# Optimization experiments

Measured on AMD Instinct MI355X. Metric: run time of the kernel, lower is better.

Reference implementation:

```python
import jax, jax.numpy as jnp
import numpy as np
from jax import lax

B, T = 2, 2048
HID = 2048
H, K, KC = 16, 128, 4
D = H * K  # projection dim
EPS = 1e-5
SCALE = K ** -0.5


def causal_conv_silu(x, w, b):
    # x: [B,T,D], depthwise causal conv, w: [D,KC], b: [D]
    xp = jnp.pad(jnp.swapaxes(x, 1, 2), ((0, 0), (0, 0), (KC - 1, 0)))  # [B,D,T+KC-1]
    y = lax.conv_general_dilated(xp, w[:, None, :], (1,), 'VALID', feature_group_count=D)
    return jax.nn.silu(jnp.swapaxes(y, 1, 2) + b)


def l2norm(x):
    return x * lax.rsqrt(jnp.sum(x * x, -1, keepdims=True) + 1e-6)


def kda_scan(q, k, v, g, beta):
    # gated delta-rule linear recurrence (KDA), per-key-dim log decay g
    # q,k,v,g: [B,T,H,K]; beta: [B,T,H]
    qT, kT, vT, gT, bT = (jnp.moveaxis(a, 1, 0) for a in (q, k, v, g, beta))
    S0 = jnp.zeros((q.shape[0], H, K, K), q.dtype)  # state [B,H,K,V]

    def step(S, inp):
        qt, kt, vt, gt, bt = inp
        S = S * jnp.exp(gt)[..., None]                                   # decay along K
        vd = (vt - jnp.einsum('bhkv,bhk->bhv', S, kt)) * bt[..., None]   # delta-rule error * beta
        S = S + kt[..., None] * vd[:, :, None, :]                        # rank-1 update
        return S, jnp.einsum('bhkv,bhk->bhv', S, qt)

    _, o = lax.scan(step, S0, (qT, kT, vT, gT, bT))
    return jnp.moveaxis(o, 0, 1)  # [B,T,H,K]


def _forward(x, Wq, Wk, Wv, conv_q_w, conv_q_b, conv_k_w, conv_k_b, conv_v_w, conv_v_b,
             Wfa, Wfb, A_log, dt_bias, Wb, Wga, Wgb, o_norm_w, Wo):
    b, t = x.shape[:2]
    q = causal_conv_silu(x @ Wq, conv_q_w, conv_q_b).reshape(b, t, H, K)
    k = causal_conv_silu(x @ Wk, conv_k_w, conv_k_b).reshape(b, t, H, K)
    v = causal_conv_silu(x @ Wv, conv_v_w, conv_v_b).reshape(b, t, H, K)
    # fine-grained decay gate: g = -exp(A_log[h]) * softplus(f_b(f_a(x)) + dt_bias)
    g = jax.nn.softplus((x @ Wfa) @ Wfb + dt_bias).reshape(b, t, H, K)
    g = -jnp.exp(A_log)[None, None, :, None] * g
    beta = jax.nn.sigmoid(x @ Wb)  # [B,T,H]
    q = l2norm(q) * SCALE
    k = l2norm(k)
    o = kda_scan(q, k, v, g, beta)  # [B,T,H,K]
    # gated head-wise RMSNorm
    gate = ((x @ Wga) @ Wgb).reshape(b, t, H, K)
    var = jnp.mean(o * o, -1, keepdims=True)
    o = o * lax.rsqrt(var + EPS) * o_norm_w * jax.nn.sigmoid(gate)
    return o.reshape(b, t, D) @ Wo


def setup_inputs() -> dict:
    key = jax.random.key(0)
    ks = jax.random.split(key, 16)
    s = 0.02
    f32 = jnp.float32
    return {
        'x': jax.random.normal(ks[0], (B, T, HID), f32),
        'Wq': jax.random.normal(ks[1], (HID, D), f32) * s,
        'Wk': jax.random.normal(ks[2], (HID, D), f32) * s,
        'Wv': jax.random.normal(ks[3], (HID, D), f32) * s,
        'conv_q_w': jax.random.normal(ks[4], (D, KC), f32) * 0.2,
        'conv_q_b': jnp.zeros((D,), f32),
        'conv_k_w': jax.random.normal(ks[5], (D, KC), f32) * 0.2,
        'conv_k_b': jnp.zeros((D,), f32),
        'conv_v_w': jax.random.normal(ks[6], (D, KC), f32) * 0.2,
        'conv_v_b': jnp.zeros((D,), f32),
        'Wfa': jax.random.normal(ks[7], (HID, K), f32) * s,
        'Wfb': jax.random.normal(ks[8], (K, D), f32) * s,
        'A_log': jnp.log(jax.random.uniform(ks[9], (H,), f32, 1.0, 16.0)),
        'dt_bias': jnp.zeros((D,), f32),
        'Wb': jax.random.normal(ks[10], (HID, H), f32) * s,
        'Wga': jax.random.normal(ks[11], (HID, K), f32) * s,
        'Wgb': jax.random.normal(ks[12], (K, D), f32) * s,
        'o_norm_w': jnp.ones((K,), f32),
        'Wo': jax.random.normal(ks[13], (D, HID), f32) * s,
    }


def reference(x, Wq, Wk, Wv, conv_q_w, conv_q_b, conv_k_w, conv_k_b, conv_v_w, conv_v_b,
              Wfa, Wfb, A_log, dt_bias, Wb, Wga, Wgb, o_norm_w, Wo):
    return _forward(x, Wq, Wk, Wv, conv_q_w, conv_q_b, conv_k_w, conv_k_b, conv_v_w, conv_v_b,
                    Wfa, Wfb, A_log, dt_bias, Wb, Wga, Wgb, o_norm_w, Wo)
```

## Files before the change

kernel.cpp:

```cpp
#include <hip/hip_runtime.h>
#include <cstddef>

#define Bsz 2
#define Tt  2048
#define HIDc 2048
#define Hh  16
#define Kc  128
#define Dc  2048
#define BT  (Bsz*Tt)
#define TS  8
#define FGBs 384

typedef __attribute__((ext_vector_type(8))) __bf16 bf16x8;
typedef __attribute__((ext_vector_type(4))) __bf16 bf16x4;
typedef __attribute__((ext_vector_type(4))) float f32x4;

__device__ __forceinline__ float epilogue(float vacc, int c, int mode,
                                          const float* __restrict__ alog,
                                          const float* __restrict__ dtb) {
    if (mode == 1) {
        float z  = vacc + dtb[c];
        float sp = fmaxf(z, 0.f) + log1pf(expf(-fabsf(z)));
        return expf(-expf(alog[c >> 7]) * sp);
    } else if (mode == 3) {
        return (c >= 256) ? 1.f / (1.f + expf(-vacc)) : vacc;
    }
    return vacc;
}

__global__ __launch_bounds__(256) void gemm_bf16_mfma(
    const __bf16* __restrict__ AB, size_t az,
    const __bf16* __restrict__ BwB, size_t bz,
    float* __restrict__ CB, size_t cz, __bf16* __restrict__ C2,
    int M, int N, int K, int lda, int mode,
    const float* __restrict__ alog, const float* __restrict__ dtb)
{
    __shared__ __bf16 As[128 * 64];
    __shared__ __bf16 Bs[128 * 64];
    const __bf16* A = AB + (size_t)blockIdx.z * az;
    const __bf16* Bw = BwB + (size_t)blockIdx.z * bz;
    float* C = CB + (size_t)blockIdx.z * cz;
    if (mode == 5) mode = (blockIdx.z == 0) ? 1 : 0;
    const int tid = threadIdx.x;
    const int lane = tid & 63;
    const int wave = tid >> 6;
    const int wr = wave >> 1, wc = wave & 1;
    const int l15 = lane & 15, g = lane >> 4;
    const int row0 = blockIdx.y * 128, col0 = blockIdx.x * 128;

    f32x4 acc[4][4];
#pragma unroll
    for (int m = 0; m < 4; m++)
#pragma unroll
        for (int n = 0; n < 4; n++)
            acc[m][n] = (f32x4){0.f, 0.f, 0.f, 0.f};

    for (int k0 = 0; k0 < K; k0 += 64) {
        __syncthreads();
#pragma unroll
        for (int i = 0; i < 4; i++) {
            const int c = i * 256 + tid;
            const int row = c >> 3, kc = c & 7;
            const int scol = k0 + 8 * (kc ^ (row & 7));
            __builtin_amdgcn_global_load_lds(
                (const __attribute__((address_space(1))) void*)(A + (size_t)(row0 + row) * lda + scol),
                (__attribute__((address_space(3))) void*)(As + (size_t)(i * 256 + (tid & ~63)) * 8),
                16, 0, 0);
        }
#pragma unroll
        for (int i = 0; i < 4; i++) {
            const int c = i * 256 + tid;
            const int row = c >> 3, kc = c & 7;
            const int scol = k0 + 8 * (kc ^ (row & 7));
            __builtin_amdgcn_global_load_lds(
                (const __attribute__((address_space(1))) void*)(Bw + (size_t)(col0 + row) * K + scol),
                (__attribute__((address_space(3))) void*)(Bs + (size_t)(i * 256 + (tid & ~63)) * 8),
                16, 0, 0);
        }
        __syncthreads();
#pragma unroll
        for (int ks = 0; ks < 2; ks++) {
            bf16x8 af[4], bfr[4];
#pragma unroll
            for (int m = 0; m < 4; m++) {
                const int row = wr * 64 + m * 16 + l15;
                const int kc = ks * 4 + g;
                af[m] = *(const bf16x8*)(As + row * 64 + 8 * (kc ^ (row & 7)));
            }
#pragma unroll
            for (int n = 0; n < 4; n++) {
                const int col = wc * 64 + n * 16 + l15;
                const int kc = ks * 4 + g;
                bfr[n] = *(const bf16x8*)(Bs + col * 64 + 8 * (kc ^ (col & 7)));
            }
#pragma unroll
            for (int m = 0; m < 4; m++)
#pragma unroll
                for (int n = 0; n < 4; n++)
                    acc[m][n] = __builtin_amdgcn_mfma_f32_16x16x32_bf16(
                        af[m], bfr[n], acc[m][n], 0, 0, 0);
        }
    }
#pragma unroll
    for (int m = 0; m < 4; m++) {
        const int rbase = row0 + wr * 64 + m * 16 + g * 4;
#pragma unroll
        for (int n = 0; n < 4; n++) {
            const int col = col0 + wc * 64 + n * 16 + l15;
#pragma unroll
            for (int r = 0; r < 4; r++) {
                const float val = epilogue(acc[m][n][r], col, mode, alog, dtb);
                C[(size_t)(rbase + r) * N + col] = val;
                if (C2) C2[(size_t)(rbase + r) * N + col] = (__bf16)val;
            }
        }
    }
}

__global__ __launch_bounds__(256) void cvt_bf16(
    const float* __restrict__ in, __bf16* __restrict__ o)
{
    const int i = blockIdx.x * 256 + threadIdx.x;
    float4 v = *(const float4*)(in + (size_t)4 * i);
    bf16x4 r;
    r[0] = (__bf16)v.x; r[1] = (__bf16)v.y; r[2] = (__bf16)v.z; r[3] = (__bf16)v.w;
    *(bf16x4*)(o + (size_t)4 * i) = r;
}

__global__ __launch_bounds__(256) void transpose_to_bf16(
    const float* __restrict__ W, __bf16* __restrict__ WT, int Kd, int N)
{
    __shared__ float tile[32][33];
    const int n0 = blockIdx.x * 32, k0 = blockIdx.y * 32;
    const int tx = threadIdx.x & 31, ty = threadIdx.x >> 5;
#pragma unroll
    for (int i = 0; i < 4; i++)
        tile[ty + 8 * i][tx] = W[(size_t)(k0 + ty + 8 * i) * N + n0 + tx];
    __syncthreads();
#pragma unroll
    for (int i = 0; i < 4; i++)
        WT[(size_t)(n0 + ty + 8 * i) * Kd + k0 + tx] = (__bf16)tile[tx][ty + 8 * i];
}

__global__ __launch_bounds__(256) void transpose3_to_bf16(
    const float* __restrict__ W0, const float* __restrict__ W1,
    const float* __restrict__ W2, __bf16* __restrict__ WTB, size_t wz,
    int Kd, int N)
{
    __shared__ float tile[32][33];
    const float* W = (blockIdx.z == 0) ? W0 : (blockIdx.z == 1) ? W1 : W2;
    __bf16* WT = WTB + (size_t)blockIdx.z * wz;
    const int n0 = blockIdx.x * 32, k0 = blockIdx.y * 32;
    const int tx = threadIdx.x & 31, ty = threadIdx.x >> 5;
#pragma unroll
    for (int i = 0; i < 4; i++)
        tile[ty + 8 * i][tx] = W[(size_t)(k0 + ty + 8 * i) * N + n0 + tx];
    __syncthreads();
#pragma unroll
    for (int i = 0; i < 4; i++)
        WT[(size_t)(n0 + ty + 8 * i) * Kd + k0 + tx] = (__bf16)tile[tx][ty + 8 * i];
}

__global__ __launch_bounds__(256) void pack_fgbT(
    const float* __restrict__ Wfa, const float* __restrict__ Wga,
    const float* __restrict__ Wb, __bf16* __restrict__ BcatT)
{
    const int i = blockIdx.x * 256 + threadIdx.x;
    if (i >= FGBs * HIDc) return;
    const int c = i / HIDc, k = i % HIDc;
    float v = 0.f;
    if (c < 128)      v = Wfa[(size_t)k * 128 + c];
    else if (c < 256) v = Wga[(size_t)k * 128 + (c - 128)];
    else if (c < 272) v = Wb[(size_t)k * 16 + (c - 256)];
    BcatT[i] = (__bf16)v;
}

__global__ __launch_bounds__(128) void conv_silu_norm(
    const float* __restrict__ pre, const float* __restrict__ cw,
    const float* __restrict__ cb, float* __restrict__ out, int mode)
{
    const int bid = blockIdx.x;
    const int h = bid & (Hh - 1);
    const int bt = bid >> 4;
    const int t = bt & (Tt - 1);
    const int lane = threadIdx.x;
    const int col = h * Kc + lane;
    const float w0 = cw[col * 4 + 0], w1 = cw[col * 4 + 1];
    const float w2 = cw[col * 4 + 2], w3 = cw[col * 4 + 3];
    const float* bp = pre + (size_t)bt * Dc + col;
    float acc = cb[col] + w3 * bp[0];
    if (t >= 1) acc += w2 * bp[-Dc];
    if (t >= 2) acc += w1 * bp[-2 * Dc];
    if (t >= 3) acc += w0 * bp[-3 * Dc];
    float val = acc / (1.f + expf(-acc));
    if (mode) {
        float ss = val * val;
#pragma unroll
        for (int m = 1; m < 64; m <<= 1) ss += __shfl_xor(ss, m);
        __shared__ float p2[2];
        if ((lane & 63) == 0) p2[lane >> 6] = ss;
        __syncthreads();
        float tot = p2[0] + p2[1];
        float r = rsqrtf(tot + 1e-6f);
        val *= r;
        if (mode == 2) val *= 0.08838834764831845f;
    }
    out[(size_t)bt * Dc + col] = val;
}

template <int CTRL>
__device__ __forceinline__ float dpp_add(float v) {
    return __int_as_float(__builtin_amdgcn_update_dpp(
        0, __float_as_int(v), CTRL, 0xf, 0xf, true));
}

__device__ __forceinline__ void reduce3_row(float& a, float& b, float& c) {
    a += dpp_add<0xB1>(a);
    b += dpp_add<0xB1>(b);
    c += dpp_add<0xB1>(c);
    a += dpp_add<0x4E>(a);
    b += dpp_add<0x4E>(b);
    c += dpp_add<0x4E>(c);
    a += dpp_add<0x124>(a);
    b += dpp_add<0x124>(b);
    c += dpp_add<0x124>(c);
    a += dpp_add<0x128>(a);
    b += dpp_add<0x128>(b);
    c += dpp_add<0x128>(c);
}

__device__ __forceinline__ float kda_step(
    const float4 cq[2], const float4 ck[2], const float4 cd[2],
    float cv, float cbt, float S[8])
{
    float kv0 = 0.f, kv1 = 0.f, qs0 = 0.f, qs1 = 0.f, qk0 = 0.f, qk1 = 0.f;
#pragma unroll
    for (int i = 0; i < 2; i++) {
        S[4 * i + 0] *= cd[i].x;
        S[4 * i + 1] *= cd[i].y;
        S[4 * i + 2] *= cd[i].z;
        S[4 * i + 3] *= cd[i].w;
        kv0 = fmaf(ck[i].x, S[4 * i + 0], kv0);
        kv1 = fmaf(ck[i].y, S[4 * i + 1], kv1);
        kv0 = fmaf(ck[i].z, S[4 * i + 2], kv0);
        kv1 = fmaf(ck[i].w, S[4 * i + 3], kv1);
        qs0 = fmaf(cq[i].x, S[4 * i + 0], qs0);
        qs1 = fmaf(cq[i].y, S[4 * i + 1], qs1);
        qs0 = fmaf(cq[i].z, S[4 * i + 2], qs0);
        qs1 = fmaf(cq[i].w, S[4 * i + 3], qs1);
        qk0 = fmaf(ck[i].x, cq[i].x, qk0);
        qk1 = fmaf(ck[i].y, cq[i].y, qk1);
        qk0 = fmaf(ck[i].z, cq[i].z, qk0);
        qk1 = fmaf(ck[i].w, cq[i].w, qk1);
    }
    float kv = kv0 + kv1, qs = qs0 + qs1, qk = qk0 + qk1;
    reduce3_row(kv, qs, qk);
    float vd = (cv - kv) * cbt;
    float ov = fmaf(qk, vd, qs);
#pragma unroll
    for (int i = 0; i < 2; i++) {
        S[4 * i + 0] = fmaf(ck[i].x, vd, S[4 * i + 0]);
        S[4 * i + 1] = fmaf(ck[i].y, vd, S[4 * i + 1]);
        S[4 * i + 2] = fmaf(ck[i].z, vd, S[4 * i + 2]);
        S[4 * i + 3] = fmaf(ck[i].w, vd, S[4 * i + 3]);
    }
    return ov;
}

__device__ __forceinline__ void kda_tile(
    const float (*sm)[TS * 128], const float* vm,
    const float* bm, float S[8], int sl0, int sl1, int vloc,
    float* __restrict__ op, int lane)
{
    float4 cq[2], ck[2], cd[2];
    float cv, cb;
    cq[0] = *(const float4*)&sm[0][sl0];
    ck[0] = *(const float4*)&sm[1][sl0];
    cd[0] = *(const float4*)&sm[2][sl0];
    cq[1] = *(const float4*)&sm[0][sl1];
    ck[1] = *(const float4*)&sm[1][sl1];
    cd[1] = *(const float4*)&sm[2][sl1];
    cv = vm[vloc];
    cb = bm[0];
#pragma unroll
    for (int t = 0; t < TS; ++t) {
        float4 nq[2], nk[2], nd[2];
        float nv = 0.f, nb = 0.f;
        if (t + 1 < TS) {
            nq[0] = *(const float4*)&sm[0][(t + 1) * 128 + sl0];
            nk[0] = *(const float4*)&sm[1][(t + 1) * 128 + sl0];
            nd[0] = *(const float4*)&sm[2][(t + 1) * 128 + sl0];
            nq[1] = *(const float4*)&sm[0][(t + 1) * 128 + sl1];
            nk[1] = *(const float4*)&sm[1][(t + 1) * 128 + sl1];
            nd[1] = *(const float4*)&sm[2][(t + 1) * 128 + sl1];
            nv = vm[(t + 1) * 4 + vloc];
            nb = bm[t + 1];
        }
        const float ov = kda_step(cq, ck, cd, cv, cb, S);
        if ((lane & 15) == 0)
            op[(size_t)t * Dc + vloc] = ov;
        if (t + 1 < TS) {
#pragma unroll
            for (int i = 0; i < 2; i++) { cq[i] = nq[i]; ck[i] = nk[i]; cd[i] = nd[i]; }
            cv = nv; cb = nb;
        }
    }
}

__global__ __launch_bounds__(64, 2) void kda_scan_kernel(
    const float* __restrict__ q, const float* __restrict__ k,
    const float* __restrict__ v, const float* __restrict__ dec,
    const float* __restrict__ fgb, float* __restrict__ o)
{
    __shared__ float sA[3][TS * 128];
    __shared__ float sB[3][TS * 128];
    __shared__ float sC[3][TS * 128];
    __shared__ float vA[TS * 4], vB[TS * 4], vC[TS * 4];
    __shared__ float bA[TS], bB[TS], bC[TS];

    const int bid = blockIdx.x;
    const int r8 = bid & 7;
    const int s = bid >> 3;
    const int bh = r8 + 8 * (s >> 5);
    const int vc = s & 31;
    const int h = bh & (Hh - 1);
    const int b = bh >> 4;
    const int lane = threadIdx.x;
    const int vloc = lane >> 4;
    const int kq = lane & 15;
    const int sl0 = ((kq * 2 + 0 + vloc) & 31) * 4;
    const int sl1 = ((kq * 2 + 1 + vloc) & 31) * 4;
    const size_t base = ((size_t)b * Tt) * Dc + h * Kc;
    const size_t bbase = ((size_t)b * Tt) * FGBs + 256 + h;

    float S[8];
#pragma unroll
    for (int i = 0; i < 8; i++) S[i] = 0.f;

    const int s_t = lane >> 5;
    const int s_w = lane & 31;

#define STAGE(TILE, SM, VM, BM)                                                 \
    {                                                                           \
        _Pragma("unroll")                                                       \
        for (int r = 0; r < 4; r++) {                                           \
            const size_t rb = base + (size_t)((TILE) * TS + 2 * r + s_t) * Dc   \
                              + s_w * 4;                                        \
            __builtin_amdgcn_global_load_lds(                                   \
                (const __attribute__((address_space(1))) void*)(q + rb),        \
                (__attribute__((address_space(3))) void*)(&SM[0][r * 256]),     \
                16, 0, 0);                                                      \
            __builtin_amdgcn_global_load_lds(                                   \
                (const __attribute__((address_space(1))) void*)(k + rb),        \
                (__attribute__((address_space(3))) void*)(&SM[1][r * 256]),     \
                16, 0, 0);                                                      \
            __builtin_amdgcn_global_load_lds(                                   \
                (const __attribute__((address_space(1))) void*)(dec + rb),      \
                (__attribute__((address_space(3))) void*)(&SM[2][r * 256]),     \
                16, 0, 0);                                                      \
        }                                                                       \
        if (lane < 32)                                                          \
            __builtin_amdgcn_global_load_lds(                                   \
                (const __attribute__((address_space(1))) void*)(v + base        \
                    + (size_t)((TILE) * TS + (lane >> 2)) * Dc + vc * 4         \
                    + (lane & 3)),                                              \
                (__attribute__((address_space(3))) void*)(&VM[0]), 4, 0, 0);    \
        if (lane < TS)                                                          \
            __builtin_amdgcn_global_load_lds(                                   \
                (const __attribute__((address_space(1))) void*)(fgb + bbase     \
                    + (size_t)((TILE) * TS + lane) * FGBs),                     \
                (__attribute__((address_space(3))) void*)(&BM[0]), 4, 0, 0);    \
    }

    STAGE(0, sA, vA, bA);
    STAGE(1, sB, vB, bB);
    asm volatile("s_waitcnt vmcnt(14)" ::: "memory");
    __builtin_amdgcn_sched_barrier(0);

    const int NT = Tt / TS;
    int cur = 0, nx2 = 2;
    for (int tile = 0; tile < NT; ++tile) {
        if (tile + 2 < NT) {
            float (*sT)[TS * 128] = (nx2 == 0) ? sA : (nx2 == 1) ? sB : sC;
            float* vT = (nx2 == 0) ? vA : (nx2 == 1) ? vB : vC;
            float* bT = (nx2 == 0) ? bA : (nx2 == 1) ? bB : bC;
            STAGE(tile + 2, sT, vT, bT);
            __builtin_amdgcn_sched_barrier(0);
        }
        const float (*sm)[TS * 128] = (cur == 0) ? sA : (cur == 1) ? sB : sC;
        const float* vm = (cur == 0) ? vA : (cur == 1) ? vB : vC;
        const float* bm = (cur == 0) ? bA : (cur == 1) ? bB : bC;
        kda_tile(sm, vm, bm, S, sl0, sl1, vloc,
                 o + base + (size_t)tile * TS * Dc + vc * 4, lane);
        if (tile + 2 < NT)
            asm volatile("s_waitcnt vmcnt(22)" ::: "memory");
        else
            asm volatile("s_waitcnt vmcnt(8)" ::: "memory");
        __builtin_amdgcn_sched_barrier(0);
        cur = (cur == 2) ? 0 : cur + 1;
        nx2 = (nx2 == 2) ? 0 : nx2 + 1;
    }
#undef STAGE
}

__global__ __launch_bounds__(128) void post_norm(
    const float* __restrict__ o, const float* __restrict__ gate,
    const float* __restrict__ onw, __bf16* __restrict__ og)
{
    const int bid = blockIdx.x;
    const int h = bid & (Hh - 1);
    const int bt = bid >> 4;
    const int lane = threadIdx.x;
    size_t idx = (size_t)bt * Dc + h * Kc + lane;
    float ov = o[idx];
    float ss = ov * ov;
#pragma unroll
    for (int m = 1; m < 64; m <<= 1) ss += __shfl_xor(ss, m);
    __shared__ float p2[2];
    if ((lane & 63) == 0) p2[lane >> 6] = ss;
    __syncthreads();
    float var = (p2[0] + p2[1]) * (1.f / 128.f);
    float r = rsqrtf(var + 1e-5f);
    float gt = gate[idx];
    og[idx] = (__bf16)(ov * r * onw[lane] * (1.f / (1.f + expf(-gt))));
}

extern "C" void kernel_launch(void* const* d_in, const int* in_sizes, int n_in,
                              void* d_out, int out_size, void* d_ws, size_t ws_size,
                              hipStream_t stream) {
    const float* x        = (const float*)d_in[0];
    const float* Wq       = (const float*)d_in[1];
    const float* Wk       = (const float*)d_in[2];
    const float* Wv       = (const float*)d_in[3];
    const float* conv_q_w = (const float*)d_in[4];
    const float* conv_q_b = (const float*)d_in[5];
    const float* conv_k_w = (const float*)d_in[6];
    const float* conv_k_b = (const float*)d_in[7];
    const float* conv_v_w = (const float*)d_in[8];
    const float* conv_v_b = (const float*)d_in[9];
    const float* Wfa      = (const float*)d_in[10];
    const float* Wfb      = (const float*)d_in[11];
    const float* A_log    = (const float*)d_in[12];
    const float* dt_bias  = (const float*)d_in[13];
    const float* Wb       = (const float*)d_in[14];
    const float* Wga      = (const float*)d_in[15];
    const float* Wgb      = (const float*)d_in[16];
    const float* o_norm_w = (const float*)d_in[17];
    const float* Wo       = (const float*)d_in[18];
    float* out = (float*)d_out;

    float* ws = (float*)d_ws;
    const size_t SZ = (size_t)BT * Dc;
    float* bufA = ws + 0 * SZ;
    float* bufB = ws + 1 * SZ;
    float* bufC = ws + 2 * SZ;
    float* bufG = ws + 3 * SZ;
    float* bufI = ws + 4 * SZ;
    float* bufQ = ws + 5 * SZ;
    float* fgb  = ws + 6 * SZ;
    __bf16* fgb16 = (__bf16*)(fgb + (size_t)BT * FGBs);
    __bf16* xb    = fgb16 + (size_t)BT * FGBs;
    __bf16* wT3   = xb + SZ;
    __bf16* BcatT = wT3 + (size_t)3 * HIDc * Dc;
    const size_t WZ = (size_t)HIDc * Dc;
    const size_t WZS = (size_t)Dc * Kc;

    dim3 blk(256);
    cvt_bf16<<<dim3(SZ / 1024), blk, 0, stream>>>(x, xb);
    pack_fgbT<<<dim3((FGBs * HIDc + 255) / 256), blk, 0, stream>>>(Wfa, Wga, Wb, BcatT);
    dim3 tgrid3(Dc / 32, HIDc / 32, 3);
    transpose3_to_bf16<<<tgrid3, blk, 0, stream>>>(Wq, Wk, Wv, wT3, WZ, HIDc, Dc);
    dim3 gbig3(Dc / 128, BT / 128, 3);
    gemm_bf16_mfma<<<gbig3, blk, 0, stream>>>(xb, 0, wT3, WZ, bufA, SZ, nullptr,
                                              BT, Dc, HIDc, HIDc, 0, nullptr, nullptr);
    dim3 gskin(FGBs / 128, BT / 128, 1);
    gemm_bf16_mfma<<<gskin, blk, 0, stream>>>(xb, 0, BcatT, 0, fgb, 0, fgb16,
                                              BT, FGBs, HIDc, HIDc, 3, nullptr, nullptr);
    dim3 tskin2(Dc / 32, Kc / 32, 2);
    transpose3_to_bf16<<<tskin2, blk, 0, stream>>>(Wfb, Wgb, Wgb, wT3, WZS, Kc, Dc);
    dim3 gdg(Dc / 128, BT / 128, 2);
    gemm_bf16_mfma<<<gdg, blk, 0, stream>>>(fgb16, 128, wT3, WZS, bufG, SZ, nullptr,
                                            BT, Dc, Kc, FGBs, 5, A_log, dt_bias);
    dim3 cblk(128);
    dim3 cgrid(BT * Hh);
    conv_silu_norm<<<cgrid, cblk, 0, stream>>>(bufA, conv_q_w, conv_q_b, bufQ, 2);
    conv_silu_norm<<<cgrid, cblk, 0, stream>>>(bufB, conv_k_w, conv_k_b, bufA, 1);
    conv_silu_norm<<<cgrid, cblk, 0, stream>>>(bufC, conv_v_w, conv_v_b, bufB, 0);
    kda_scan_kernel<<<dim3(1024), dim3(64), 0, stream>>>(bufQ, bufA, bufB, bufG, fgb, bufC);
    post_norm<<<cgrid, cblk, 0, stream>>>(bufC, bufI, o_norm_w, xb);
    dim3 tgrid(Dc / 32, HIDc / 32);
    transpose_to_bf16<<<tgrid, blk, 0, stream>>>(Wo, wT3, Dc, HIDc);
    dim3 gout(HIDc / 128, BT / 128, 1);
    gemm_bf16_mfma<<<gout, blk, 0, stream>>>(xb, 0, wT3, 0, out, 0, nullptr,
                                             BT, HIDc, Dc, Dc, 0, nullptr, nullptr);
}
```

Before: 912.8 us.

## Split KDA scan across twice as many blocks with 2 value columns each

```diff
diff --git a/kernel.cpp b/kernel.cpp
--- a/kernel.cpp
+++ b/kernel.cpp
@@ -8,7 +8,7 @@
 #define Kc  128
 #define Dc  2048
 #define BT  (Bsz*Tt)
-#define TS  8
+#define TS  4
 #define FGBs 384
 
 typedef __attribute__((ext_vector_type(8))) __bf16 bf16x8;
@@ -214,7 +214,17 @@
         0, __float_as_int(v), CTRL, 0xf, 0xf, true));
 }
 
-__device__ __forceinline__ void reduce3_row(float& a, float& b, float& c) {
+__device__ __forceinline__ float sum_x16(float v) {
+#if __has_builtin(__builtin_amdgcn_permlane16_swap)
+    auto r = __builtin_amdgcn_permlane16_swap(__float_as_uint(v), __float_as_uint(v),
+                                              false, false);
+    return __uint_as_float(r[0]) + __uint_as_float(r[1]);
+#else
+    return v + __shfl_xor(v, 16);
+#endif
+}
+
+__device__ __forceinline__ void reduce3_32(float& a, float& b, float& c) {
     a += dpp_add<0xB1>(a);
     b += dpp_add<0xB1>(b);
     c += dpp_add<0xB1>(c);
@@ -227,82 +237,71 @@
     a += dpp_add<0x128>(a);
     b += dpp_add<0x128>(b);
     c += dpp_add<0x128>(c);
+    a = sum_x16(a);
+    b = sum_x16(b);
+    c = sum_x16(c);
 }
 
 __device__ __forceinline__ float kda_step(
-    const float4 cq[2], const float4 ck[2], const float4 cd[2],
-    float cv, float cbt, float S[8])
-{
+    const float4 cq, const float4 ck, const float4 cd,
+    float cv, float cbt, float S[4])
+{
+    S[0] *= cd.x;
+    S[1] *= cd.y;
+    S[2] *= cd.z;
+    S[3] *= cd.w;
     float kv0 = 0.f, kv1 = 0.f, qs0 = 0.f, qs1 = 0.f, qk0 = 0.f, qk1 = 0.f;
-#pragma unroll
-    for (int i = 0; i < 2; i++) {
-        S[4 * i + 0] *= cd[i].x;
-        S[4 * i + 1] *= cd[i].y;
-        S[4 * i + 2] *= cd[i].z;
-        S[4 * i + 3] *= cd[i].w;
-        kv0 = fmaf(ck[i].x, S[4 * i + 0], kv0);
-        kv1 = fmaf(ck[i].y, S[4 * i + 1], kv1);
-        kv0 = fmaf(ck[i].z, S[4 * i + 2], kv0);
-        kv1 = fmaf(ck[i].w, S[4 * i + 3], kv1);
-        qs0 = fmaf(cq[i].x, S[4 * i + 0], qs0);
-        qs1 = fmaf(cq[i].y, S[4 * i + 1], qs1);
-        qs0 = fmaf(cq[i].z, S[4 * i + 2], qs0);
-        qs1 = fmaf(cq[i].w, S[4 * i + 3], qs1);
-        qk0 = fmaf(ck[i].x, cq[i].x, qk0);
-        qk1 = fmaf(ck[i].y, cq[i].y, qk1);
-        qk0 = fmaf(ck[i].z, cq[i].z, qk0);
-        qk1 = fmaf(ck[i].w, cq[i].w, qk1);
-    }
+    kv0 = fmaf(ck.x, S[0], kv0);
+    kv1 = fmaf(ck.y, S[1], kv1);
+    kv0 = fmaf(ck.z, S[2], kv0);
+    kv1 = fmaf(ck.w, S[3], kv1);
+    qs0 = fmaf(cq.x, S[0], qs0);
+    qs1 = fmaf(cq.y, S[1], qs1);
+    qs0 = fmaf(cq.z, S[2], qs0);
+    qs1 = fmaf(cq.w, S[3], qs1);
+    qk0 = fmaf(ck.x, cq.x, qk0);
+    qk1 = fmaf(ck.y, cq.y, qk1);
+    qk0 = fmaf(ck.z, cq.z, qk0);
+    qk1 = fmaf(ck.w, cq.w, qk1);
     float kv = kv0 + kv1, qs = qs0 + qs1, qk = qk0 + qk1;
-    reduce3_row(kv, qs, qk);
+    reduce3_32(kv, qs, qk);
     float vd = (cv - kv) * cbt;
     float ov = fmaf(qk, vd, qs);
-#pragma unroll
-    for (int i = 0; i < 2; i++) {
-        S[4 * i + 0] = fmaf(ck[i].x, vd, S[4 * i + 0]);
-        S[4 * i + 1] = fmaf(ck[i].y, vd, S[4 * i + 1]);
-        S[4 * i + 2] = fmaf(ck[i].z, vd, S[4 * i + 2]);
-        S[4 * i + 3] = fmaf(ck[i].w, vd, S[4 * i + 3]);
-    }
+    S[0] = fmaf(ck.x, vd, S[0]);
+    S[1] = fmaf(ck.y, vd, S[1]);
+    S[2] = fmaf(ck.z, vd, S[2]);
+    S[3] = fmaf(ck.w, vd, S[3]);
     return ov;
 }
 
 __device__ __forceinline__ void kda_tile(
     const float (*sm)[TS * 128], const float* vm,
-    const float* bm, float S[8], int sl0, int sl1, int vloc,
+    const float* bm, float S[4], int kq, int vloc,
     float* __restrict__ op, int lane)
 {
-    float4 cq[2], ck[2], cd[2];
+    float4 cq, ck, cd;
     float cv, cb;
-    cq[0] = *(const float4*)&sm[0][sl0];
-    ck[0] = *(const float4*)&sm[1][sl0];
-    cd[0] = *(const float4*)&sm[2][sl0];
-    cq[1] = *(const float4*)&sm[0][sl1];
-    ck[1] = *(const float4*)&sm[1][sl1];
-    cd[1] = *(const float4*)&sm[2][sl1];
+    cq = *(const float4*)&sm[0][kq * 4];
+    ck = *(const float4*)&sm[1][kq * 4];
+    cd = *(const float4*)&sm[2][kq * 4];
     cv = vm[vloc];
     cb = bm[0];
 #pragma unroll
     for (int t = 0; t < TS; ++t) {
-        float4 nq[2], nk[2], nd[2];
+        float4 nq, nk, nd;
         float nv = 0.f, nb = 0.f;
         if (t + 1 < TS) {
-            nq[0] = *(const float4*)&sm[0][(t + 1) * 128 + sl0];
-            nk[0] = *(const float4*)&sm[1][(t + 1) * 128 + sl0];
-            nd[0] = *(const float4*)&sm[2][(t + 1) * 128 + sl0];
-            nq[1] = *(const float4*)&sm[0][(t + 1) * 128 + sl1];
-            nk[1] = *(const float4*)&sm[1][(t + 1) * 128 + sl1];
-            nd[1] = *(const float4*)&sm[2][(t + 1) * 128 + sl1];
-            nv = vm[(t + 1) * 4 + vloc];
+            nq = *(const float4*)&sm[0][(t + 1) * 128 + kq * 4];
+            nk = *(const float4*)&sm[1][(t + 1) * 128 + kq * 4];
+            nd = *(const float4*)&sm[2][(t + 1) * 128 + kq * 4];
+            nv = vm[(t + 1) * 2 + vloc];
             nb = bm[t + 1];
         }
         const float ov = kda_step(cq, ck, cd, cv, cb, S);
-        if ((lane & 15) == 0)
+        if ((lane & 31) == 0)
             op[(size_t)t * Dc + vloc] = ov;
         if (t + 1 < TS) {
-#pragma unroll
-            for (int i = 0; i < 2; i++) { cq[i] = nq[i]; ck[i] = nk[i]; cd[i] = nd[i]; }
-            cv = nv; cb = nb;
+            cq = nq; ck = nk; cd = nd; cv = nv; cb = nb;
         }
     }
 }
@@ -315,27 +314,25 @@
     __shared__ float sA[3][TS * 128];
     __shared__ float sB[3][TS * 128];
     __shared__ float sC[3][TS * 128];
-    __shared__ float vA[TS * 4], vB[TS * 4], vC[TS * 4];
+    __shared__ float vA[TS * 2], vB[TS * 2], vC[TS * 2];
     __shared__ float bA[TS], bB[TS], bC[TS];
 
     const int bid = blockIdx.x;
     const int r8 = bid & 7;
     const int s = bid >> 3;
-    const int bh = r8 + 8 * (s >> 5);
-    const int vc = s & 31;
+    const int bh = r8 + 8 * (s >> 6);
+    const int vc = s & 63;
     const int h = bh & (Hh - 1);
     const int b = bh >> 4;
     const int lane = threadIdx.x;
-    const int vloc = lane >> 4;
-    const int kq = lane & 15;
-    const int sl0 = ((kq * 2 + 0 + vloc) & 31) * 4;
-    const int sl1 = ((kq * 2 + 1 + vloc) & 31) * 4;
+    const int vloc = lane >> 5;
+    const int kq = lane & 31;
     const size_t base = ((size_t)b * Tt) * Dc + h * Kc;
     const size_t bbase = ((size_t)b * Tt) * FGBs + 256 + h;
 
-    float S[8];
-#pragma unroll
-    for (int i = 0; i < 8; i++) S[i] = 0.f;
+    float S[4];
+#pragma unroll
+    for (int i = 0; i < 4; i++) S[i] = 0.f;
 
     const int s_t = lane >> 5;
     const int s_w = lane & 31;
@@ -343,7 +340,7 @@
 #define STAGE(TILE, SM, VM, BM)                                                 \
     {                                                                           \
         _Pragma("unroll")                                                       \
-        for (int r = 0; r < 4; r++) {                                           \
+        for (int r = 0; r < 2; r++) {                                           \
             const size_t rb = base + (size_t)((TILE) * TS + 2 * r + s_t) * Dc   \
                               + s_w * 4;                                        \
             __builtin_amdgcn_global_load_lds(                                   \
@@ -359,11 +356,11 @@
                 (__attribute__((address_space(3))) void*)(&SM[2][r * 256]),     \
                 16, 0, 0);                                                      \
         }                                                                       \
-        if (lane < 32)                                                          \
+        if (lane < 2 * TS)                                                      \
             __builtin_amdgcn_global_load_lds(                                   \
                 (const __attribute__((address_space(1))) void*)(v + base        \
-                    + (size_t)((TILE) * TS + (lane >> 2)) * Dc + vc * 4         \
-                    + (lane & 3)),                                              \
+                    + (size_t)((TILE) * TS + (lane >> 1)) * Dc + vc * 2         \
+                    + (lane & 1)),                                              \
                 (__attribute__((address_space(3))) void*)(&VM[0]), 4, 0, 0);    \
         if (lane < TS)                                                          \
             __builtin_amdgcn_global_load_lds(                                   \
@@ -374,7 +371,7 @@
 
     STAGE(0, sA, vA, bA);
     STAGE(1, sB, vB, bB);
-    asm volatile("s_waitcnt vmcnt(14)" ::: "memory");
+    asm volatile("s_waitcnt vmcnt(8)" ::: "memory");
     __builtin_amdgcn_sched_barrier(0);
 
     const int NT = Tt / TS;
@@ -390,12 +387,12 @@
         const float (*sm)[TS * 128] = (cur == 0) ? sA : (cur == 1) ? sB : sC;
         const float* vm = (cur == 0) ? vA : (cur == 1) ? vB : vC;
         const float* bm = (cur == 0) ? bA : (cur == 1) ? bB : bC;
-        kda_tile(sm, vm, bm, S, sl0, sl1, vloc,
-                 o + base + (size_t)tile * TS * Dc + vc * 4, lane);
+        kda_tile(sm, vm, bm, S, kq, vloc,
+                 o + base + (size_t)tile * TS * Dc + vc * 2, lane);
         if (tile + 2 < NT)
-            asm volatile("s_waitcnt vmcnt(22)" ::: "memory");
+            asm volatile("s_waitcnt vmcnt(12)" ::: "memory");
         else
-            asm volatile("s_waitcnt vmcnt(8)" ::: "memory");
+            asm volatile("s_waitcnt vmcnt(4)" ::: "memory");
         __builtin_amdgcn_sched_barrier(0);
         cur = (cur == 2) ? 0 : cur + 1;
         nx2 = (nx2 == 2) ? 0 : nx2 + 1;
@@ -486,7 +483,7 @@
     conv_silu_norm<<<cgrid, cblk, 0, stream>>>(bufA, conv_q_w, conv_q_b, bufQ, 2);
     conv_silu_norm<<<cgrid, cblk, 0, stream>>>(bufB, conv_k_w, conv_k_b, bufA, 1);
     conv_silu_norm<<<cgrid, cblk, 0, stream>>>(bufC, conv_v_w, conv_v_b, bufB, 0);
-    kda_scan_kernel<<<dim3(1024), dim3(64), 0, stream>>>(bufQ, bufA, bufB, bufG, fgb, bufC);
+    kda_scan_kernel<<<dim3(2048), dim3(64), 0, stream>>>(bufQ, bufA, bufB, bufG, fgb, bufC);
     post_norm<<<cgrid, cblk, 0, stream>>>(bufC, bufI, o_norm_w, xb);
     dim3 tgrid(Dc / 32, HIDc / 32);
     transpose_to_bf16<<<tgrid, blk, 0, stream>>>(Wo, wT3, Dc, HIDc);
```

Result: slower. 1.034 ms (+13.2%).

## Process two value columns per lane in KDA scan, halving blocks

Applied to the files above, without the earlier changes.

```diff
diff --git a/kernel.cpp b/kernel.cpp
--- a/kernel.cpp
+++ b/kernel.cpp
@@ -214,78 +214,105 @@
         0, __float_as_int(v), CTRL, 0xf, 0xf, true));
 }
 
-__device__ __forceinline__ void reduce3_row(float& a, float& b, float& c) {
+__device__ __forceinline__ void reduce5_row(float& a, float& b, float& c,
+                                            float& d, float& e) {
     a += dpp_add<0xB1>(a);
     b += dpp_add<0xB1>(b);
     c += dpp_add<0xB1>(c);
+    d += dpp_add<0xB1>(d);
+    e += dpp_add<0xB1>(e);
     a += dpp_add<0x4E>(a);
     b += dpp_add<0x4E>(b);
     c += dpp_add<0x4E>(c);
+    d += dpp_add<0x4E>(d);
+    e += dpp_add<0x4E>(e);
     a += dpp_add<0x124>(a);
     b += dpp_add<0x124>(b);
     c += dpp_add<0x124>(c);
+    d += dpp_add<0x124>(d);
+    e += dpp_add<0x124>(e);
     a += dpp_add<0x128>(a);
     b += dpp_add<0x128>(b);
     c += dpp_add<0x128>(c);
-}
-
-__device__ __forceinline__ float kda_step(
+    d += dpp_add<0x128>(d);
+    e += dpp_add<0x128>(e);
+}
+
+__device__ __forceinline__ void kda_step2(
     const float4 cq[2], const float4 ck[2], const float4 cd[2],
-    float cv, float cbt, float S[8])
-{
-    float kv0 = 0.f, kv1 = 0.f, qs0 = 0.f, qs1 = 0.f, qk0 = 0.f, qk1 = 0.f;
+    float cva, float cvb, float cbt, float Sa[8], float Sb[8],
+    float& ova, float& ovb)
+{
+    float kva = 0.f, kvb = 0.f, qsa = 0.f, qsb = 0.f, qk = 0.f;
 #pragma unroll
     for (int i = 0; i < 2; i++) {
-        S[4 * i + 0] *= cd[i].x;
-        S[4 * i + 1] *= cd[i].y;
-        S[4 * i + 2] *= cd[i].z;
-        S[4 * i + 3] *= cd[i].w;
-        kv0 = fmaf(ck[i].x, S[4 * i + 0], kv0);
-        kv1 = fmaf(ck[i].y, S[4 * i + 1], kv1);
-        kv0 = fmaf(ck[i].z, S[4 * i + 2], kv0);
-        kv1 = fmaf(ck[i].w, S[4 * i + 3], kv1);
-        qs0 = fmaf(cq[i].x, S[4 * i + 0], qs0);
-        qs1 = fmaf(cq[i].y, S[4 * i + 1], qs1);
-        qs0 = fmaf(cq[i].z, S[4 * i + 2], qs0);
-        qs1 = fmaf(cq[i].w, S[4 * i + 3], qs1);
-        qk0 = fmaf(ck[i].x, cq[i].x, qk0);
-        qk1 = fmaf(ck[i].y, cq[i].y, qk1);
-        qk0 = fmaf(ck[i].z, cq[i].z, qk0);
-        qk1 = fmaf(ck[i].w, cq[i].w, qk1);
-    }
-    float kv = kv0 + kv1, qs = qs0 + qs1, qk = qk0 + qk1;
-    reduce3_row(kv, qs, qk);
-    float vd = (cv - kv) * cbt;
-    float ov = fmaf(qk, vd, qs);
+        Sa[4 * i + 0] *= cd[i].x;
+        Sa[4 * i + 1] *= cd[i].y;
+        Sa[4 * i + 2] *= cd[i].z;
+        Sa[4 * i + 3] *= cd[i].w;
+        Sb[4 * i + 0] *= cd[i].x;
+        Sb[4 * i + 1] *= cd[i].y;
+        Sb[4 * i + 2] *= cd[i].z;
+        Sb[4 * i + 3] *= cd[i].w;
+        kva = fmaf(ck[i].x, Sa[4 * i + 0], kva);
+        kva = fmaf(ck[i].y, Sa[4 * i + 1], kva);
+        kva = fmaf(ck[i].z, Sa[4 * i + 2], kva);
+        kva = fmaf(ck[i].w, Sa[4 * i + 3], kva);
+        kvb = fmaf(ck[i].x, Sb[4 * i + 0], kvb);
+        kvb = fmaf(ck[i].y, Sb[4 * i + 1], kvb);
+        kvb = fmaf(ck[i].z, Sb[4 * i + 2], kvb);
+        kvb = fmaf(ck[i].w, Sb[4 * i + 3], kvb);
+        qsa = fmaf(cq[i].x, Sa[4 * i + 0], qsa);
+        qsa = fmaf(cq[i].y, Sa[4 * i + 1], qsa);
+        qsa = fmaf(cq[i].z, Sa[4 * i + 2], qsa);
+        qsa = fmaf(cq[i].w, Sa[4 * i + 3], qsa);
+        qsb = fmaf(cq[i].x, Sb[4 * i + 0], qsb);
+        qsb = fmaf(cq[i].y, Sb[4 * i + 1], qsb);
+        qsb = fmaf(cq[i].z, Sb[4 * i + 2], qsb);
+        qsb = fmaf(cq[i].w, Sb[4 * i + 3], qsb);
+        qk = fmaf(ck[i].x, cq[i].x, qk);
+        qk = fmaf(ck[i].y, cq[i].y, qk);
+        qk = fmaf(ck[i].z, cq[i].z, qk);
+        qk = fmaf(ck[i].w, cq[i].w, qk);
+    }
+    reduce5_row(kva, kvb, qsa, qsb, qk);
+    const float vda = (cva - kva) * cbt;
+    const float vdb = (cvb - kvb) * cbt;
+    ova = fmaf(qk, vda, qsa);
+    ovb = fmaf(qk, vdb, qsb);
 #pragma unroll
     for (int i = 0; i < 2; i++) {
-        S[4 * i + 0] = fmaf(ck[i].x, vd, S[4 * i + 0]);
-        S[4 * i + 1] = fmaf(ck[i].y, vd, S[4 * i + 1]);
-        S[4 * i + 2] = fmaf(ck[i].z, vd, S[4 * i + 2]);
-        S[4 * i + 3] = fmaf(ck[i].w, vd, S[4 * i + 3]);
-    }
-    return ov;
-}
-
-__device__ __forceinline__ void kda_tile(
+        Sa[4 * i + 0] = fmaf(ck[i].x, vda, Sa[4 * i + 0]);
+        Sa[4 * i + 1] = fmaf(ck[i].y, vda, Sa[4 * i + 1]);
+        Sa[4 * i + 2] = fmaf(ck[i].z, vda, Sa[4 * i + 2]);
+        Sa[4 * i + 3] = fmaf(ck[i].w, vda, Sa[4 * i + 3]);
+        Sb[4 * i + 0] = fmaf(ck[i].x, vdb, Sb[4 * i + 0]);
+        Sb[4 * i + 1] = fmaf(ck[i].y, vdb, Sb[4 * i + 1]);
+        Sb[4 * i + 2] = fmaf(ck[i].z, vdb, Sb[4 * i + 2]);
+        Sb[4 * i + 3] = fmaf(ck[i].w, vdb, Sb[4 * i + 3]);
+    }
+}
+
+__device__ __forceinline__ void kda_tile2(
     const float (*sm)[TS * 128], const float* vm,
-    const float* bm, float S[8], int sl0, int sl1, int vloc,
+    const float* bm, float Sa[8], float Sb[8], int sl0, int sl1, int vloc,
     float* __restrict__ op, int lane)
 {
     float4 cq[2], ck[2], cd[2];
-    float cv, cb;
+    float cva, cvb, cb;
     cq[0] = *(const float4*)&sm[0][sl0];
     ck[0] = *(const float4*)&sm[1][sl0];
     cd[0] = *(const float4*)&sm[2][sl0];
     cq[1] = *(const float4*)&sm[0][sl1];
     ck[1] = *(const float4*)&sm[1][sl1];
     cd[1] = *(const float4*)&sm[2][sl1];
-    cv = vm[vloc];
+    cva = vm[vloc];
+    cvb = vm[4 + vloc];
     cb = bm[0];
 #pragma unroll
     for (int t = 0; t < TS; ++t) {
         float4 nq[2], nk[2], nd[2];
-        float nv = 0.f, nb = 0.f;
+        float nva = 0.f, nvb = 0.f, nb = 0.f;
         if (t + 1 < TS) {
             nq[0] = *(const float4*)&sm[0][(t + 1) * 128 + sl0];
             nk[0] = *(const float4*)&sm[1][(t + 1) * 128 + sl0];
@@ -293,16 +320,20 @@
             nq[1] = *(const float4*)&sm[0][(t + 1) * 128 + sl1];
             nk[1] = *(const float4*)&sm[1][(t + 1) * 128 + sl1];
             nd[1] = *(const float4*)&sm[2][(t + 1) * 128 + sl1];
-            nv = vm[(t + 1) * 4 + vloc];
+            nva = vm[(t + 1) * 8 + vloc];
+            nvb = vm[(t + 1) * 8 + 4 + vloc];
             nb = bm[t + 1];
         }
-        const float ov = kda_step(cq, ck, cd, cv, cb, S);
-        if ((lane & 15) == 0)
-            op[(size_t)t * Dc + vloc] = ov;
+        float ova, ovb;
+        kda_step2(cq, ck, cd, cva, cvb, cb, Sa, Sb, ova, ovb);
+        if ((lane & 15) == 0) {
+            op[(size_t)t * Dc + vloc] = ova;
+            op[(size_t)t * Dc + 4 + vloc] = ovb;
+        }
         if (t + 1 < TS) {
 #pragma unroll
             for (int i = 0; i < 2; i++) { cq[i] = nq[i]; ck[i] = nk[i]; cd[i] = nd[i]; }
-            cv = nv; cb = nb;
+            cva = nva; cvb = nvb; cb = nb;
         }
     }
 }
@@ -315,14 +346,14 @@
     __shared__ float sA[3][TS * 128];
     __shared__ float sB[3][TS * 128];
     __shared__ float sC[3][TS * 128];
-    __shared__ float vA[TS * 4], vB[TS * 4], vC[TS * 4];
+    __shared__ float vA[TS * 8], vB[TS * 8], vC[TS * 8];
     __shared__ float bA[TS], bB[TS], bC[TS];
 
     const int bid = blockIdx.x;
     const int r8 = bid & 7;
     const int s = bid >> 3;
-    const int bh = r8 + 8 * (s >> 5);
-    const int vc = s & 31;
+    const int bh = r8 + 8 * (s >> 4);
+    const int vc = s & 15;
     const int h = bh & (Hh - 1);
     const int b = bh >> 4;
     const int lane = threadIdx.x;
@@ -333,12 +364,14 @@
     const size_t base = ((size_t)b * Tt) * Dc + h * Kc;
     const size_t bbase = ((size_t)b * Tt) * FGBs + 256 + h;
 
-    float S[8];
-#pragma unroll
-    for (int i = 0; i < 8; i++) S[i] = 0.f;
+    float Sa[8], Sb[8];
+#pragma unroll
+    for (int i = 0; i < 8; i++) { Sa[i] = 0.f; Sb[i] = 0.f; }
 
     const int s_t = lane >> 5;
     const int s_w = lane & 31;
+    const int v_t = lane >> 3;
+    const int v_j = lane & 7;
 
 #define STAGE(TILE, SM, VM, BM)                                                 \
     {                                                                           \
@@ -359,12 +392,10 @@
                 (__attribute__((address_space(3))) void*)(&SM[2][r * 256]),     \
                 16, 0, 0);                                                      \
         }                                                                       \
-        if (lane < 32)                                                          \
-            __builtin_amdgcn_global_load_lds(                                   \
-                (const __attribute__((address_space(1))) void*)(v + base        \
-                    + (size_t)((TILE) * TS + (lane >> 2)) * Dc + vc * 4         \
-                    + (lane & 3)),                                              \
-                (__attribute__((address_space(3))) void*)(&VM[0]), 4, 0, 0);    \
+        __builtin_amdgcn_global_load_lds(                                       \
+            (const __attribute__((address_space(1))) void*)(v + base            \
+                + (size_t)((TILE) * TS + v_t) * Dc + vc * 8 + v_j),             \
+            (__attribute__((address_space(3))) void*)(&VM[0]), 4, 0, 0);        \
         if (lane < TS)                                                          \
             __builtin_amdgcn_global_load_lds(                                   \
                 (const __attribute__((address_space(1))) void*)(fgb + bbase     \
@@ -390,12 +421,12 @@
         const float (*sm)[TS * 128] = (cur == 0) ? sA : (cur == 1) ? sB : sC;
         const float* vm = (cur == 0) ? vA : (cur == 1) ? vB : vC;
         const float* bm = (cur == 0) ? bA : (cur == 1) ? bB : bC;
-        kda_tile(sm, vm, bm, S, sl0, sl1, vloc,
-                 o + base + (size_t)tile * TS * Dc + vc * 4, lane);
+        kda_tile2(sm, vm, bm, Sa, Sb, sl0, sl1, vloc,
+                  o + base + (size_t)tile * TS * Dc + vc * 8, lane);
         if (tile + 2 < NT)
-            asm volatile("s_waitcnt vmcnt(22)" ::: "memory");
+            asm volatile("s_waitcnt vmcnt(30)" ::: "memory");
         else
-            asm volatile("s_waitcnt vmcnt(8)" ::: "memory");
+            asm volatile("s_waitcnt vmcnt(16)" ::: "memory");
         __builtin_amdgcn_sched_barrier(0);
         cur = (cur == 2) ? 0 : cur + 1;
         nx2 = (nx2 == 2) ? 0 : nx2 + 1;
@@ -486,7 +517,7 @@
     conv_silu_norm<<<cgrid, cblk, 0, stream>>>(bufA, conv_q_w, conv_q_b, bufQ, 2);
     conv_silu_norm<<<cgrid, cblk, 0, stream>>>(bufB, conv_k_w, conv_k_b, bufA, 1);
     conv_silu_norm<<<cgrid, cblk, 0, stream>>>(bufC, conv_v_w, conv_v_b, bufB, 0);
-    kda_scan_kernel<<<dim3(1024), dim3(64), 0, stream>>>(bufQ, bufA, bufB, bufG, fgb, bufC);
+    kda_scan_kernel<<<dim3(512), dim3(64), 0, stream>>>(bufQ, bufA, bufB, bufG, fgb, bufC);
     post_norm<<<cgrid, cblk, 0, stream>>>(bufC, bufI, o_norm_w, xb);
     dim3 tgrid(Dc / 32, HIDc / 32);
     transpose_to_bf16<<<tgrid, blk, 0, stream>>>(Wo, wT3, Dc, HIDc);
```

Measured after the change: 1.057 ms. +15.8%, slower.
